# Optimization experiments

Hardware: AMD Instinct MI355X
Metric: run time of the kernel (lower is better)

The kernel has to match this reference:

```python
import jax, jax.numpy as jnp
import numpy as np

N_EDGES = 30000
K = 8                 # ragged width (Kmax)
N_TRIP = N_EDGES * K  # 240000
EMB = 128             # emb_size
INTERM = 64           # emb_size_interm
SPH = 16              # num_spherical
UNITS_OUT = 128


def setup_inputs() -> dict:
    key = jax.random.key(0)
    k1, k2, k3, k4 = jax.random.split(key, 4)
    rbf_W1 = jax.random.normal(k1, (N_EDGES, INTERM, SPH), dtype=jnp.float32)
    sph = jax.random.normal(k2, (N_EDGES, SPH, K), dtype=jnp.float32)
    m = jax.random.normal(k3, (N_TRIP, EMB), dtype=jnp.float32)
    # he_orthogonal_init ~ zero-mean, var 1/fan_in with fan_in = EMB*INTERM
    fan_in = EMB * INTERM
    weight = jax.random.normal(k4, (EMB, INTERM, UNITS_OUT), dtype=jnp.float32) * (1.0 / fan_in) ** 0.5
    # deterministic ragged layout: each edge owns exactly K consecutive triplets
    idx = jnp.arange(N_TRIP, dtype=jnp.int64 if jax.config.jax_enable_x64 else jnp.int32)
    id_reduce = idx // K
    id_ragged_idx = idx % K
    return {
        "rbf_W1": rbf_W1,
        "sph": sph,
        "m": m,
        "weight": weight,
        "id_reduce": id_reduce,
        "id_ragged_idx": id_ragged_idx,
        "Kmax": K,
    }


def reference(rbf_W1, sph, m, weight, id_reduce, id_ragged_idx, Kmax):
    nEdges = rbf_W1.shape[0]
    emb = m.shape[1]
    # ragged scatter-assign: m2[id_reduce, id_ragged_idx] = m
    m2 = jnp.zeros((nEdges, Kmax, emb), dtype=m.dtype)
    m2 = m2.at[id_reduce, id_ragged_idx].set(m)
    # sum_k = sph @ m2 : (E, S, K) x (E, K, H) -> (E, S, H)
    sum_k = jnp.einsum("esk,ekh->esh", sph, m2)
    # rbf_W1_sum_k = rbf_W1 @ sum_k : (E, I, S) x (E, S, H) -> (E, I, H)
    rbf_W1_sum_k = jnp.einsum("eis,esh->eih", rbf_W1, sum_k)
    # bilinear contraction + sum over H: (E, I, H) x (H, I, O) -> (E, O)
    m_ca = jnp.einsum("eih,hio->eo", rbf_W1_sum_k, weight)
    return m_ca
```

## Files before the change

kernel.cpp:

```cpp
#include <hip/hip_runtime.h>
#include <stdint.h>


#define EMB 128
#define INTERM 64
#define SPH_N 16
#define KMAX 8
#define OUTD 128
#define KDIM 8192
#define EB 64
#define NTHR 512
#define NCHUNK 256

typedef __attribute__((ext_vector_type(8))) __fp16 f16x8;
typedef __attribute__((ext_vector_type(2))) __fp16 f16x2;
typedef __attribute__((ext_vector_type(4))) float f32x4;
typedef __attribute__((ext_vector_type(4))) int i32x4;

#if defined(__has_builtin)
#if __has_builtin(__builtin_amdgcn_fdot2)
#define HAVE_FDOT2 1
#endif
#endif
#ifndef HAVE_FDOT2
#define HAVE_FDOT2 0
#endif

__device__ __forceinline__ unsigned short f32_to_f16u(float f) {
  union { f16x2 h; uint32_t u; } c; c.h = __builtin_amdgcn_cvt_pkrtz(f, f);
  return (unsigned short)(c.u & 0xffffu);
}
__device__ __forceinline__ uint32_t pk_f16(float lo, float hi) {
  union { f16x2 h; uint32_t u; } c; c.h = __builtin_amdgcn_cvt_pkrtz(lo, hi);
  return c.u;
}
__device__ __forceinline__ f16x8 as_h16(f32x4 v) {
  union { f32x4 f; f16x8 h; } u; u.f = v; return u.h;
}
__device__ __forceinline__ float dot2(f16x2 a, f16x2 b, float c) {
#if HAVE_FDOT2
  return __builtin_amdgcn_fdot2(a, b, c, false);
#else
  return c + (float)a[0] * (float)b[0] + (float)a[1] * (float)b[1];
#endif
}
__device__ __forceinline__ void gload_bv(f32x4& d, const unsigned short* sbase, uint32_t voff) {
  asm volatile("global_load_dwordx4 %0, %1, %2" : "=&v"(d) : "v"(voff), "s"(sbase));
}

__global__ void k_build_inv(const int* __restrict__ id_reduce,
                            const int* __restrict__ id_ragged,
                            int* __restrict__ inv, int nTrip, int E) {
  int t = blockIdx.x * blockDim.x + threadIdx.x;
  if (t >= nTrip) return;
  int e = id_reduce[t], k = id_ragged[t];
  if (e >= 0 && e < E && k >= 0 && k < KMAX) inv[e * KMAX + k] = t;
}

__global__ void k_w2t(const float* __restrict__ W, unsigned short* __restrict__ W2T) {
  int idx = blockIdx.x * blockDim.x + threadIdx.x;
  int o = idx >> 13;
  int c = idx & (KDIM - 1);
  int h = c & 127, i = c >> 7;
  W2T[idx] = f32_to_f16u(W[(h * INTERM + i) * OUTD + o]);
}

__global__ void k_spht(const float* __restrict__ sph, float* __restrict__ sphT, int E) {
  int idx = blockIdx.x * blockDim.x + threadIdx.x;
  int e = idx >> 7, r = idx & 127;
  if (e >= E) return;
  int k = r >> 4, s = r & 15;
  sphT[(size_t)e * 128 + k * 16 + s] = sph[(size_t)e * 128 + s * 8 + k];
}

__global__ __launch_bounds__(NTHR, 2) void k_fused(
    const float* __restrict__ rbf,
    const float* __restrict__ sphT,
    const float* __restrict__ m,
    const int* __restrict__ inv,
    const unsigned short* __restrict__ W2T,
    float* __restrict__ out, int E)
{
  __shared__ unsigned short s_rs[EB * 64 * 8];
  __shared__ unsigned short s_A[2][2][EB * 32];

  int tid = threadIdx.x;
  int e0 = blockIdx.x * EB;
  int eL = tid >> 3;
  int kq = tid & 7;
  int hq = kq;
  int eg = e0 + eL;
  bool ev = (eg < E);
  int esw8 = (eL & 7) << 3;
  int asw  = (eL & 3) << 3;

  {
    f32x4 sp0 = 0.f, sp1 = 0.f, sp2 = 0.f, sp3 = 0.f;
    if (ev) {
      const f32x4* sp = (const f32x4*)(sphT + (size_t)eg * 128 + kq * 16);
      sp0 = sp[0]; sp1 = sp[1]; sp2 = sp[2]; sp3 = sp[3];
    }
    const f32x4* rb = (const f32x4*)(rbf + (size_t)eg * 1024);
#pragma unroll 4
    for (int i = 0; i < 64; ++i) {
      float v = 0.f;
      if (ev) {
        f32x4 q0 = rb[i * 4 + 0], q1 = rb[i * 4 + 1];
        f32x4 q2 = rb[i * 4 + 2], q3 = rb[i * 4 + 3];
        v = q0.x * sp0.x + q0.y * sp0.y + q0.z * sp0.z + q0.w * sp0.w
          + q1.x * sp1.x + q1.y * sp1.y + q1.z * sp1.z + q1.w * sp1.w
          + q2.x * sp2.x + q2.y * sp2.y + q2.z * sp2.z + q2.w * sp2.w
          + q3.x * sp3.x + q3.y * sp3.y + q3.z * sp3.z + q3.w * sp3.w;
      }
      s_rs[(eL << 9) + (((i << 3) ^ esw8) | kq)] = f32_to_f16u(v);
    }
  }

  int wid = tid >> 6, lane = tid & 63;
  int lr = lane & 15, lg = lane >> 4;
  int aidx0 = ((0 * 16 + lr) << 5) + ((lg << 3) ^ ((lr & 3) << 3));
  int aidx1 = ((1 * 16 + lr) << 5) + ((lg << 3) ^ ((lr & 3) << 3));
  int aidx2 = ((2 * 16 + lr) << 5) + ((lg << 3) ^ ((lr & 3) << 3));
  int aidx3 = ((3 * 16 + lr) << 5) + ((lg << 3) ^ ((lr & 3) << 3));
  uint32_t voff = (uint32_t)((((wid * 16 + lr) * KDIM) + lg * 8) * 2);

  f16x2 m2p[4][4];

#define LOAD_M2(HW)                                                              \
  {                                                                              \
    i32x4 iv0, iv1;                                                              \
    const int* ip_ = inv + (size_t)eg * 8;                                       \
    asm volatile("global_load_dwordx4 %0, %1, off" : "=&v"(iv0) : "v"(ip_));     \
    asm volatile("global_load_dwordx4 %0, %1, off" : "=&v"(iv1) : "v"(ip_ + 4)); \
    asm volatile("s_waitcnt vmcnt(0)" : "+v"(iv0), "+v"(iv1));                   \
    int tk_[8] = {iv0.x, iv0.y, iv0.z, iv0.w, iv1.x, iv1.y, iv1.z, iv1.w};       \
    f32x4 mm_[8];                                                                \
    _Pragma("unroll")                                                            \
    for (int k = 0; k < 8; ++k) {                                                \
      const float* mp_ = m + (size_t)(tk_[k] < 0 ? 0 : tk_[k]) * EMB             \
                         + (HW) * 32 + hq * 4;                                   \
      asm volatile("global_load_dwordx4 %0, %1, off" : "=&v"(mm_[k]) : "v"(mp_));\
    }                                                                            \
    asm volatile("s_waitcnt vmcnt(0)"                                            \
                 : "+v"(mm_[0]), "+v"(mm_[1]), "+v"(mm_[2]), "+v"(mm_[3]),       \
                   "+v"(mm_[4]), "+v"(mm_[5]), "+v"(mm_[6]), "+v"(mm_[7]));      \
    _Pragma("unroll")                                                            \
    for (int k = 0; k < 8; ++k)                                                  \
      if (tk_[k] < 0) mm_[k] = (f32x4){0.f, 0.f, 0.f, 0.f};                      \
    _Pragma("unroll")                                                            \
    for (int d = 0; d < 4; ++d) {                                                \
      _Pragma("unroll")                                                          \
      for (int kp = 0; kp < 4; ++kp)                                             \
        m2p[d][kp] = __builtin_amdgcn_cvt_pkrtz(mm_[2 * kp][d], mm_[2 * kp + 1][d]); \
    }                                                                            \
  }

#define PRODUCE(RR, PAR, SL)                                                 \
  {                                                                          \
    union { uint4 u; f16x2 p[4]; } rsu; rsu.u = (RR);                        \
    float a0 = 0.f, a1 = 0.f, a2 = 0.f, a3 = 0.f;                            \
    _Pragma("unroll")                                                        \
    for (int kp = 0; kp < 4; ++kp) {                                         \
      a0 = dot2(rsu.p[kp], m2p[0][kp], a0);                                  \
      a1 = dot2(rsu.p[kp], m2p[1][kp], a1);                                  \
      a2 = dot2(rsu.p[kp], m2p[2][kp], a2);                                  \
      a3 = dot2(rsu.p[kp], m2p[3][kp], a3);                                  \
    }                                                                        \
    uint32_t p0 = pk_f16(a0, a1), p1 = pk_f16(a2, a3);                       \
    *(uint2*)&s_A[PAR][SL][(eL << 5) + ((hq << 2) ^ asw)] =                  \
        make_uint2(p0, p1);                                                  \
  }

  f32x4 acc0 = {0.f, 0.f, 0.f, 0.f}, acc1 = acc0, acc2 = acc0, acc3 = acc0;
  f32x4 bvA, bvB;
  uint4 rsA0, rsA1, rsB0, rsB1;

  LOAD_M2(0)
  {
    uint4 rs0 = *(const uint4*)&s_rs[(eL << 9) + esw8];
    uint4 rs1 = *(const uint4*)&s_rs[(eL << 9) + ((1 << 3) ^ esw8)];
    PRODUCE(rs0, 0, 0)
    PRODUCE(rs1, 0, 1)
  }
  rsA0 = *(const uint4*)&s_rs[(eL << 9) + ((2 << 3) ^ esw8)];
  rsA1 = *(const uint4*)&s_rs[(eL << 9) + ((3 << 3) ^ esw8)];
  gload_bv(bvA, W2T + 0, voff);
  gload_bv(bvB, W2T + 128, voff);
  asm volatile("s_waitcnt lgkmcnt(0)" ::: "memory");
  __builtin_amdgcn_s_barrier();

#define PERIOD(P, PAR, RSP0, RSP1, RSF0, RSF1, M2CHK, PROD, PF, W1S, W2S)        \
  {                                                                              \
    const int c_ = 2 * (P);                                                      \
    f16x8 a00 = *(const f16x8*)&s_A[PAR][0][aidx0];                              \
    f16x8 a01 = *(const f16x8*)&s_A[PAR][0][aidx1];                              \
    f16x8 a02 = *(const f16x8*)&s_A[PAR][0][aidx2];                              \
    f16x8 a03 = *(const f16x8*)&s_A[PAR][0][aidx3];                              \
    f16x8 a10 = *(const f16x8*)&s_A[PAR][1][aidx0];                              \
    f16x8 a11 = *(const f16x8*)&s_A[PAR][1][aidx1];                              \
    f16x8 a12 = *(const f16x8*)&s_A[PAR][1][aidx2];                              \
    f16x8 a13 = *(const f16x8*)&s_A[PAR][1][aidx3];                              \
    if (PF) {                                                                    \
      RSF0 = *(const uint4*)&s_rs[(eL << 9) + ((((c_ + 4) & 63) << 3) ^ esw8)];  \
      RSF1 = *(const uint4*)&s_rs[(eL << 9) + ((((c_ + 5) & 63) << 3) ^ esw8)];  \
    }                                                                            \
    if (M2CHK && (((c_ + 2) & 63) == 0)) LOAD_M2((c_ + 2) >> 6)                  \
    if (PROD) { PRODUCE(RSP0, (PAR) ^ 1, 0) PRODUCE(RSP1, (PAR) ^ 1, 1) }        \
    asm volatile(W1S : "+v"(bvA));                                               \
    {                                                                            \
      f16x8 bvv = as_h16(bvA);                                                   \
      acc0 = __builtin_amdgcn_mfma_f32_16x16x32_f16(a00, bvv, acc0, 0, 0, 0);    \
      acc1 = __builtin_amdgcn_mfma_f32_16x16x32_f16(a01, bvv, acc1, 0, 0, 0);    \
      acc2 = __builtin_amdgcn_mfma_f32_16x16x32_f16(a02, bvv, acc2, 0, 0, 0);    \
      acc3 = __builtin_amdgcn_mfma_f32_16x16x32_f16(a03, bvv, acc3, 0, 0, 0);    \
    }                                                                            \
    if (PF) {                                                                    \
      uint32_t wo_ = (uint32_t)((((c_ + 2) & 63) << 7) + (((c_ + 2) >> 6) << 5));\
      gload_bv(bvA, W2T + wo_, voff);                                            \
    }                                                                            \
    asm volatile(W2S : "+v"(bvB));                                               \
    {                                                                            \
      f16x8 bvv = as_h16(bvB);                                                   \
      acc0 = __builtin_amdgcn_mfma_f32_16x16x32_f16(a10, bvv, acc0, 0, 0, 0);    \
      acc1 = __builtin_amdgcn_mfma_f32_16x16x32_f16(a11, bvv, acc1, 0, 0, 0);    \
      acc2 = __builtin_amdgcn_mfma_f32_16x16x32_f16(a12, bvv, acc2, 0, 0, 0);    \
      acc3 = __builtin_amdgcn_mfma_f32_16x16x32_f16(a13, bvv, acc3, 0, 0, 0);    \
    }                                                                            \
    if (PF) {                                                                    \
      uint32_t wo_ = (uint32_t)((((c_ + 3) & 63) << 7) + (((c_ + 3) >> 6) << 5));\
      gload_bv(bvB, W2T + wo_, voff);                                            \
    }                                                                            \
    asm volatile("s_waitcnt lgkmcnt(0)" ::: "memory");                           \
    __builtin_amdgcn_s_barrier();                                                \
  }

  for (int p = 0; p < 126; p += 2) {
    PERIOD(p,     0, rsA0, rsA1, rsB0, rsB1, 1, 1, 1,
           "s_waitcnt vmcnt(1)", "s_waitcnt vmcnt(1)")
    PERIOD(p + 1, 1, rsB0, rsB1, rsA0, rsA1, 1, 1, 1,
           "s_waitcnt vmcnt(1)", "s_waitcnt vmcnt(1)")
  }
  PERIOD(126, 0, rsA0, rsA1, rsB0, rsB1, 0, 1, 1,
         "s_waitcnt vmcnt(1)", "s_waitcnt vmcnt(1)")
  PERIOD(127, 1, rsB0, rsB1, rsA0, rsA1, 0, 0, 0,
         "s_waitcnt vmcnt(1)", "s_waitcnt vmcnt(0)")

  {
    int col = wid * 16 + lr;
#pragma unroll
    for (int r = 0; r < 4; ++r) {
      int rb_ = e0 + lg * 4 + r;
      if (rb_ + 0 < E)  out[(size_t)(rb_ + 0)  * OUTD + col] = acc0[r];
      if (rb_ + 16 < E) out[(size_t)(rb_ + 16) * OUTD + col] = acc1[r];
      if (rb_ + 32 < E) out[(size_t)(rb_ + 32) * OUTD + col] = acc2[r];
      if (rb_ + 48 < E) out[(size_t)(rb_ + 48) * OUTD + col] = acc3[r];
    }
  }
}

extern "C" void kernel_launch(void* const* d_in, const int* in_sizes, int n_in,
                              void* d_out, int out_size, void* d_ws, size_t ws_size,
                              hipStream_t stream) {
  const float* rbf = (const float*)d_in[0];
  const float* sph = (const float*)d_in[1];
  const float* m   = (const float*)d_in[2];
  const float* W   = (const float*)d_in[3];
  const int* id_reduce = (const int*)d_in[4];
  const int* id_ragged = (const int*)d_in[5];
  float* out = (float*)d_out;

  int E = in_sizes[0] / (INTERM * SPH_N);
  int nTrip = in_sizes[2] / EMB;
  int nblk = (E + EB - 1) / EB;
  int Epad = nblk * EB;

  char* ws = (char*)d_ws;
  int* inv = (int*)ws;
  unsigned short* W2T = (unsigned short*)(ws + (1u << 20));
  float* sphT = (float*)(ws + (3u << 20));

  (void)hipMemsetAsync(inv, 0xFF, (size_t)Epad * KMAX * sizeof(int), stream);
  k_build_inv<<<(nTrip + 255) / 256, 256, 0, stream>>>(id_reduce, id_ragged, inv, nTrip, E);
  k_w2t<<<(OUTD * KDIM) / 256, 256, 0, stream>>>(W, W2T);
  k_spht<<<(E * 128 + 255) / 256, 256, 0, stream>>>(sph, sphT, E);

  k_fused<<<nblk, NTHR, 0, stream>>>(rbf, sphT, m, inv, W2T, out, E);
}
```

Before: 207.9 us.

## Re-tile MFMA warp grid to 2x4 with 32x32 per-wave output tiles

Changes the per-wave MFMA tile from 64 edges by 16 output columns to 32 edges by 32 columns, using a 2x4 wave grid (ew, ow). Each wave now loads two B fragments per K-step and half as many A fragments from LDS, cutting LDS reads of the A tile. The global W loads per wave double, and the pipelined vmcnt(1) waits become a single vmcnt(0) that waits for all four prefetched B fragments. That wait shortens load/compute overlap.

```diff
diff --git a/kernel.cpp b/kernel.cpp
--- a/kernel.cpp
+++ b/kernel.cpp
@@ -118,11 +118,12 @@
 
   int wid = tid >> 6, lane = tid & 63;
   int lr = lane & 15, lg = lane >> 4;
-  int aidx0 = ((0 * 16 + lr) << 5) + ((lg << 3) ^ ((lr & 3) << 3));
-  int aidx1 = ((1 * 16 + lr) << 5) + ((lg << 3) ^ ((lr & 3) << 3));
-  int aidx2 = ((2 * 16 + lr) << 5) + ((lg << 3) ^ ((lr & 3) << 3));
-  int aidx3 = ((3 * 16 + lr) << 5) + ((lg << 3) ^ ((lr & 3) << 3));
-  uint32_t voff = (uint32_t)((((wid * 16 + lr) * KDIM) + lg * 8) * 2);
+  int ew = wid >> 2, ow = wid & 3;
+  int aidx0 = ((ew * 32 + lr) << 5) + ((lg << 3) ^ ((lr & 3) << 3));
+  int aidx1 = aidx0 + (16 << 5);
+  uint32_t voff0 = (uint32_t)((((ow * 32 + lr) * KDIM) + lg * 8) * 2);
+  uint32_t voff1 = voff0 + (uint32_t)(16 * KDIM * 2);
+#define WBASE(N) (W2T + (((N) & 63) * 128 + (((N) >> 6) << 5)))
 
   f16x2 m2p[4][4];
 
@@ -171,8 +172,8 @@
         make_uint2(p0, p1);                                                  \
   }
 
-  f32x4 acc0 = {0.f, 0.f, 0.f, 0.f}, acc1 = acc0, acc2 = acc0, acc3 = acc0;
-  f32x4 bvA, bvB;
+  f32x4 acc00 = {0.f, 0.f, 0.f, 0.f}, acc01 = acc00, acc10 = acc00, acc11 = acc00;
+  f32x4 bvA0, bvA1, bvB0, bvB1;
   uint4 rsA0, rsA1, rsB0, rsB1;
 
   LOAD_M2(0)
@@ -184,76 +185,73 @@
   }
   rsA0 = *(const uint4*)&s_rs[(eL << 9) + ((2 << 3) ^ esw8)];
   rsA1 = *(const uint4*)&s_rs[(eL << 9) + ((3 << 3) ^ esw8)];
-  gload_bv(bvA, W2T + 0, voff);
-  gload_bv(bvB, W2T + 128, voff);
+  gload_bv(bvA0, WBASE(0), voff0);
+  gload_bv(bvA1, WBASE(0), voff1);
+  gload_bv(bvB0, WBASE(1), voff0);
+  gload_bv(bvB1, WBASE(1), voff1);
   asm volatile("s_waitcnt lgkmcnt(0)" ::: "memory");
   __builtin_amdgcn_s_barrier();
 
-#define PERIOD(P, PAR, RSP0, RSP1, RSF0, RSF1, M2CHK, PROD, PF, W1S, W2S)        \
+#define PERIOD(P, PAR, RSP0, RSP1, RSF0, RSF1, M2CHK, PROD, PF)                  \
   {                                                                              \
     const int c_ = 2 * (P);                                                      \
     f16x8 a00 = *(const f16x8*)&s_A[PAR][0][aidx0];                              \
     f16x8 a01 = *(const f16x8*)&s_A[PAR][0][aidx1];                              \
-    f16x8 a02 = *(const f16x8*)&s_A[PAR][0][aidx2];                              \
-    f16x8 a03 = *(const f16x8*)&s_A[PAR][0][aidx3];                              \
     f16x8 a10 = *(const f16x8*)&s_A[PAR][1][aidx0];                              \
     f16x8 a11 = *(const f16x8*)&s_A[PAR][1][aidx1];                              \
-    f16x8 a12 = *(const f16x8*)&s_A[PAR][1][aidx2];                              \
-    f16x8 a13 = *(const f16x8*)&s_A[PAR][1][aidx3];                              \
     if (PF) {                                                                    \
       RSF0 = *(const uint4*)&s_rs[(eL << 9) + ((((c_ + 4) & 63) << 3) ^ esw8)];  \
       RSF1 = *(const uint4*)&s_rs[(eL << 9) + ((((c_ + 5) & 63) << 3) ^ esw8)];  \
     }                                                                            \
     if (M2CHK && (((c_ + 2) & 63) == 0)) LOAD_M2((c_ + 2) >> 6)                  \
     if (PROD) { PRODUCE(RSP0, (PAR) ^ 1, 0) PRODUCE(RSP1, (PAR) ^ 1, 1) }        \
-    asm volatile(W1S : "+v"(bvA));                                               \
+                  \
+    asm volatile("s_waitcnt vmcnt(0)"                                            \
+                 : "+v"(bvA0), "+v"(bvA1), "+v"(bvB0), "+v"(bvB1));              \
     {                                                                            \
-      f16x8 bvv = as_h16(bvA);                                                   \
-      acc0 = __builtin_amdgcn_mfma_f32_16x16x32_f16(a00, bvv, acc0, 0, 0, 0);    \
-      acc1 = __builtin_amdgcn_mfma_f32_16x16x32_f16(a01, bvv, acc1, 0, 0, 0);    \
-      acc2 = __builtin_amdgcn_mfma_f32_16x16x32_f16(a02, bvv, acc2, 0, 0, 0);    \
-      acc3 = __builtin_amdgcn_mfma_f32_16x16x32_f16(a03, bvv, acc3, 0, 0, 0);    \
-    }                                                                            \
+      f16x8 b0 = as_h16(bvA0), b1 = as_h16(bvA1);                                \
+      acc00 = __builtin_amdgcn_mfma_f32_16x16x32_f16(a00, b0, acc00, 0, 0, 0);   \
+      acc01 = __builtin_amdgcn_mfma_f32_16x16x32_f16(a00, b1, acc01, 0, 0, 0);   \
+      acc10 = __builtin_amdgcn_mfma_f32_16x16x32_f16(a01, b0, acc10, 0, 0, 0);   \
+      acc11 = __builtin_amdgcn_mfma_f32_16x16x32_f16(a01, b1, acc11, 0, 0, 0);   \
+      f16x8 c0 = as_h16(bvB0), c1 = as_h16(bvB1);                                \
+      acc00 = __builtin_amdgcn_mfma_f32_16x16x32_f16(a10, c0, acc00, 0, 0, 0);   \
+      acc01 = __builtin_amdgcn_mfma_f32_16x16x32_f16(a10, c1, acc01, 0, 0, 0);   \
+      acc10 = __builtin_amdgcn_mfma_f32_16x16x32_f16(a11, c0, acc10, 0, 0, 0);   \
+      acc11 = __builtin_amdgcn_mfma_f32_16x16x32_f16(a11, c1, acc11, 0, 0, 0);   \
+    }                                                                            \
+                         \
     if (PF) {                                                                    \
-      uint32_t wo_ = (uint32_t)((((c_ + 2) & 63) << 7) + (((c_ + 2) >> 6) << 5));\
-      gload_bv(bvA, W2T + wo_, voff);                                            \
-    }                                                                            \
-    asm volatile(W2S : "+v"(bvB));                                               \
-    {                                                                            \
-      f16x8 bvv = as_h16(bvB);                                                   \
-      acc0 = __builtin_amdgcn_mfma_f32_16x16x32_f16(a10, bvv, acc0, 0, 0, 0);    \
-      acc1 = __builtin_amdgcn_mfma_f32_16x16x32_f16(a11, bvv, acc1, 0, 0, 0);    \
-      acc2 = __builtin_amdgcn_mfma_f32_16x16x32_f16(a12, bvv, acc2, 0, 0, 0);    \
-      acc3 = __builtin_amdgcn_mfma_f32_16x16x32_f16(a13, bvv, acc3, 0, 0, 0);    \
-    }                                                                            \
-    if (PF) {                                                                    \
-      uint32_t wo_ = (uint32_t)((((c_ + 3) & 63) << 7) + (((c_ + 3) >> 6) << 5));\
-      gload_bv(bvB, W2T + wo_, voff);                                            \
+      gload_bv(bvA0, WBASE(c_ + 2), voff0);                                      \
+      gload_bv(bvA1, WBASE(c_ + 2), voff1);                                      \
+      gload_bv(bvB0, WBASE(c_ + 3), voff0);                                      \
+      gload_bv(bvB1, WBASE(c_ + 3), voff1);                                      \
     }                                                                            \
     asm volatile("s_waitcnt lgkmcnt(0)" ::: "memory");                           \
     __builtin_amdgcn_s_barrier();                                                \
   }
 
   for (int p = 0; p < 126; p += 2) {
-    PERIOD(p,     0, rsA0, rsA1, rsB0, rsB1, 1, 1, 1,
-           "s_waitcnt vmcnt(1)", "s_waitcnt vmcnt(1)")
-    PERIOD(p + 1, 1, rsB0, rsB1, rsA0, rsA1, 1, 1, 1,
-           "s_waitcnt vmcnt(1)", "s_waitcnt vmcnt(1)")
-  }
-  PERIOD(126, 0, rsA0, rsA1, rsB0, rsB1, 0, 1, 1,
-         "s_waitcnt vmcnt(1)", "s_waitcnt vmcnt(1)")
-  PERIOD(127, 1, rsB0, rsB1, rsA0, rsA1, 0, 0, 0,
-         "s_waitcnt vmcnt(1)", "s_waitcnt vmcnt(0)")
+    PERIOD(p,     0, rsA0, rsA1, rsB0, rsB1, 1, 1, 1)
+    PERIOD(p + 1, 1, rsB0, rsB1, rsA0, rsA1, 1, 1, 1)
+  }
+  PERIOD(126, 0, rsA0, rsA1, rsB0, rsB1, 0, 1, 1)
+  PERIOD(127, 1, rsB0, rsB1, rsA0, rsA1, 0, 0, 0)
 
   {
-    int col = wid * 16 + lr;
+    int col0 = ow * 32 + lr, col1 = col0 + 16;
+    int rbase = e0 + ew * 32 + lg * 4;
 #pragma unroll
     for (int r = 0; r < 4; ++r) {
-      int rb_ = e0 + lg * 4 + r;
-      if (rb_ + 0 < E)  out[(size_t)(rb_ + 0)  * OUTD + col] = acc0[r];
-      if (rb_ + 16 < E) out[(size_t)(rb_ + 16) * OUTD + col] = acc1[r];
-      if (rb_ + 32 < E) out[(size_t)(rb_ + 32) * OUTD + col] = acc2[r];
-      if (rb_ + 48 < E) out[(size_t)(rb_ + 48) * OUTD + col] = acc3[r];
+      int rA = rbase + r, rB = rbase + 16 + r;
+      if (rA < E) {
+        out[(size_t)rA * OUTD + col0] = acc00[r];
+        out[(size_t)rA * OUTD + col1] = acc01[r];
+      }
+      if (rB < E) {
+        out[(size_t)rB * OUTD + col0] = acc10[r];
+        out[(size_t)rB * OUTD + col1] = acc11[r];
+      }
     }
   }
 }
```

New measurement: 316.8 us. 1.52x slower.
